# Optimization experiments

Measured on AMD Instinct MI355X. Metric: run time of the kernel, lower is better.

Reference implementation:

```python
import jax, jax.numpy as jnp
import numpy as np

PAD = 8192          # padding index == bloom_filter_dim
H1, H2 = 512, 64
B, K, L = 32, 32, 128


def prelu(x, alpha):
    return jnp.where(x >= 0, x, alpha * x)


def embedding_bag_mean(w, idx):
    # EmbeddingBag(mode='mean', padding_idx=PAD): mean over non-padding entries
    emb = w[idx]                                   # [..., L, H1]
    m = (idx != PAD)[..., None].astype(w.dtype)    # [..., L, 1]
    s = (emb * m).sum(axis=-2)
    cnt = m.sum(axis=-2)
    return jnp.where(cnt > 0, s / jnp.maximum(cnt, 1.0), 0.0)


def hidden_layers(x, W1, b1, W2, b2, a0, a1, a2):
    # PReLU -> Linear -> PReLU -> Linear -> PReLU
    h = prelu(x, a0)
    h = prelu(h @ W1 + b1, a1)
    h = prelu(h @ W2 + b2, a2)
    return h


def setup_inputs() -> dict:
    key = jax.random.key(0)
    ks = jax.random.split(key, 16)
    f = lambda i, shape: jax.random.normal(ks[i], shape, dtype=jnp.float32) * 0.05
    s = lambda v: jnp.asarray(v, dtype=jnp.float32)
    return {
        'query_bloom_filter': jax.random.randint(ks[0], (B, L), 0, PAD),
        'poi_bloom_filter': jax.random.randint(ks[1], (B, K, L), 0, PAD),
        'query_loc': jax.random.normal(ks[2], (B, 2), dtype=jnp.float32),
        'poi_loc': jax.random.normal(ks[3], (B, K, 2), dtype=jnp.float32),
        'codebook_w': f(4, (PAD + 1, H1)),
        'q_W1': f(5, (H1, H2)), 'q_b1': f(6, (H2,)),
        'q_W2': f(7, (H2, H2)), 'q_b2': f(8, (H2,)),
        'p_W1': f(9, (H1, H2)), 'p_b1': f(10, (H2,)),
        'p_W2': f(11, (H2, H2)), 'p_b2': f(12, (H2,)),
        'q_eval_w': f(13, (PAD + 1, H2)),
        'p_eval_w': f(14, (PAD + 1, H2)),
        'q_a0': s(0.25), 'q_a1': s(0.25), 'q_a2': s(0.25),
        'p_a0': s(0.25), 'p_a1': s(0.25), 'p_a2': s(0.25),
        'ind_a': s(0.25),
        'a': s(1.0), 'b': s(0.0), 'c': s(1.0), 'd': s(0.0),
    }


def reference(query_bloom_filter, poi_bloom_filter, query_loc, poi_loc,
              codebook_w, q_W1, q_b1, q_W2, q_b2, p_W1, p_b1, p_W2, p_b2,
              q_eval_w, p_eval_w, q_a0, q_a1, q_a2, p_a0, p_a1, p_a2,
              ind_a, a, b, c, d):
    # --- dense towers ---
    query_embedding = embedding_bag_mean(codebook_w, query_bloom_filter)      # [B, H1]
    query_hidden = hidden_layers(query_embedding, q_W1, q_b1, q_W2, q_b2,
                                 q_a0, q_a1, q_a2)                            # [B, H2]
    poi_embedding = embedding_bag_mean(codebook_w, poi_bloom_filter)          # [B, K, H1]
    poi_hidden = hidden_layers(poi_embedding, p_W1, p_b1, p_W2, p_b2,
                               p_a0, p_a1, p_a2)                              # [B, K, H2]

    # --- bloom-filter intersection (isin_cuda): q element present in poi set ---
    q = query_bloom_filter[:, None, :]                                        # [B, 1, L]
    p = poi_bloom_filter                                                      # [B, K, L]
    match = (q[..., :, None] == p[..., None, :]) & (p[..., None, :] != PAD)   # [B, K, L, L]
    intersection_mask = match.any(axis=-1)                                    # [B, K, L]
    intersection = jnp.where(intersection_mask, q, PAD)                       # [B, K, L]

    # --- sparse term weights via evaluator gathers + mul-sum ---
    q_cols = q_eval_w[intersection]                                           # [B, K, L, H2]
    p_cols = p_eval_w[intersection]                                           # [B, K, L, H2]
    q_sw = prelu(jnp.einsum('bh,bklh->bkl', query_hidden, q_cols), ind_a) + 1.0
    p_sw = prelu(jnp.einsum('bkh,bklh->bkl', poi_hidden, p_cols), ind_a) + 1.0

    text_sim = jnp.where(intersection_mask, q_sw * p_sw, 0.0).sum(axis=-1)    # [B, K]

    # --- location similarity ---
    dist = jnp.sqrt(((query_loc[:, None, :] - poi_loc) ** 2).sum(axis=-1))    # [B, K]
    dist_sim = -jnp.log(dist + 1.0)

    # --- text-sim normalization + relevance ---
    max_sim = text_sim.max(axis=-1, keepdims=True)
    text_sim = (2.0 * text_sim - max_sim) / (max_sim + 1e-6)
    relevance_score = (c - jax.nn.sigmoid(a * text_sim + b)) * (dist_sim - d)
    return relevance_score
```

## Files before the change

kernel.cpp:

```cpp
#include <hip/hip_runtime.h>

#define PAD_V 8192
#define H1 512
#define H2 64
#define B_SZ 32
#define K_SZ 32
#define L_SZ 128
#define NBAGS (B_SZ + B_SZ * K_SZ)
#define NSLICE 8
#define GATHER_BLOCKS (NBAGS * NSLICE)
#define ISECT2_BLOCKS ((B_SZ * K_SZ) / 2)


__global__ __launch_bounds__(256, 4) void gather_kernel(
    const int* __restrict__ qbf, const int* __restrict__ pbf,
    const float* __restrict__ codebook,
    const float* __restrict__ qa0p, const float* __restrict__ pa0p,
    float* __restrict__ x_ws,
    int* __restrict__ nh_ws, int* __restrict__ hits_ws)
{
    const int tid = threadIdx.x;

    if (blockIdx.x >= GATHER_BLOCKS) {
        __shared__ unsigned int bm2[2][256];
        __shared__ int s_nh2[2];
        __shared__ int s_hit2[2][L_SZ];

        const int pair0 = (blockIdx.x - GATHER_BLOCKS) * 2;
        const int sub = tid >> 7;
        const int t   = tid & 127;
        const int pair = pair0 + sub;
        const int b = pair >> 5;

        bm2[sub][t] = 0u; bm2[sub][t + 128] = 0u;
        if (t == 0) s_nh2[sub] = 0;
        __syncthreads();

        int pv = pbf[pair * L_SZ + t];
        if ((unsigned)pv < (unsigned)PAD_V)
            atomicOr(&bm2[sub][pv >> 5], 1u << (pv & 31));
        __syncthreads();

        int v = qbf[b * L_SZ + t];
        bool hit = ((unsigned)v < (unsigned)PAD_V) &&
                   ((bm2[sub][v >> 5] >> (v & 31)) & 1u);
        if (hit) {
            int pos = atomicAdd(&s_nh2[sub], 1);
            s_hit2[sub][pos] = v;
        }
        __syncthreads();

        if (t == 0) nh_ws[pair] = s_nh2[sub];
        if (t < s_nh2[sub]) hits_ws[pair * L_SZ + t] = s_hit2[sub][t];
        return;
    }

    const int slice = blockIdx.x & (NSLICE - 1);
    const int bag   = blockIdx.x >> 3;
    const bool is_q = (bag < B_SZ);
    const int* idx_base = is_q ? qbf : pbf;
    const int  bagl     = is_q ? bag : (bag - B_SZ);
    const float a0      = is_q ? *qa0p : *pa0p;

    __shared__ int   s_idx[L_SZ];
    __shared__ int   s_cnt[2];
    __shared__ float4 s_part[16][16];

    if (tid < L_SZ) {
        int v = idx_base[bagl * L_SZ + tid];
        s_idx[tid] = v;
        unsigned long long bal = __ballot(v != PAD_V);
        if ((tid & 63) == 0) s_cnt[tid >> 6] = __popcll(bal);
    }
    __syncthreads();

    const int c  = tid & 15;
    const int r0 = tid >> 4;
    const int gc = slice * 16 + c;
    const float4* cb4 = (const float4*)codebook;

    float ax = 0.f, ay = 0.f, az = 0.f, aw = 0.f;
    {
        int    idx[8];
        float4 buf[8];
        #pragma unroll
        for (int j = 0; j < 8; j++) idx[j] = s_idx[r0 * 8 + j];
        #pragma unroll
        for (int j = 0; j < 8; j++) buf[j] = cb4[(size_t)idx[j] * 128 + gc];
        #pragma unroll
        for (int j = 0; j < 8; j++) {
            float m = (idx[j] != PAD_V) ? 1.0f : 0.0f;
            ax = fmaf(m, buf[j].x, ax);
            ay = fmaf(m, buf[j].y, ay);
            az = fmaf(m, buf[j].z, az);
            aw = fmaf(m, buf[j].w, aw);
        }
    }
    s_part[r0][c] = make_float4(ax, ay, az, aw);
    __syncthreads();

    if (tid < 16) {
        int cnt = s_cnt[0] + s_cnt[1];
        float inv = (cnt > 0) ? 1.0f / (float)cnt : 0.0f;
        float e0 = 0.f, e1 = 0.f, e2 = 0.f, e3 = 0.f;
        #pragma unroll
        for (int r = 0; r < 16; r++) {
            float4 p = s_part[r][tid];
            e0 += p.x; e1 += p.y; e2 += p.z; e3 += p.w;
        }
        e0 *= inv; e1 *= inv; e2 *= inv; e3 *= inv;
        float4 o;
        o.x = (e0 >= 0.f) ? e0 : a0 * e0;
        o.y = (e1 >= 0.f) ? e1 : a0 * e1;
        o.z = (e2 >= 0.f) ? e2 : a0 * e2;
        o.w = (e3 >= 0.f) ? e3 : a0 * e3;
        ((float4*)x_ws)[(size_t)bag * 128 + slice * 16 + tid] = o;
    }
}

__global__ __launch_bounds__(256, 8) void mlp_kernel(
    const float* __restrict__ x_ws,
    const float* __restrict__ qW1, const float* __restrict__ qb1,
    const float* __restrict__ qW2, const float* __restrict__ qb2,
    const float* __restrict__ pW1, const float* __restrict__ pb1,
    const float* __restrict__ pW2, const float* __restrict__ pb2,
    const float* __restrict__ qa1p, const float* __restrict__ qa2p,
    const float* __restrict__ pa1p, const float* __restrict__ pa2p,
    float* __restrict__ qh_out, float* __restrict__ ph_out)
{
    const int tid = threadIdx.x;
    const int bag = blockIdx.x;
    const bool is_q = (bag < B_SZ);
    const float *W1, *b1, *W2, *b2;
    float a1, a2;
    float* out;
    int bagl;
    if (is_q) {
        bagl = bag;
        W1 = qW1; b1 = qb1; W2 = qW2; b2 = qb2;
        a1 = *qa1p; a2 = *qa2p;
        out = qh_out;
    } else {
        bagl = bag - B_SZ;
        W1 = pW1; b1 = pb1; W2 = pW2; b2 = pb2;
        a1 = *pa1p; a2 = *pa2p;
        out = ph_out;
    }

    __shared__ float s_x[H1];
    __shared__ float s_p1[16][H2];
    __shared__ float s_h1[H2];

    if (tid < 128)
        ((float4*)s_x)[tid] = ((const float4*)x_ws)[(size_t)bag * 128 + tid];
    __syncthreads();

    const int j4 = tid & 15;
    const int ch = tid >> 4;

    {
        const float4* W1v = (const float4*)W1;
        const int i0 = ch * 32;
        float sx = 0.f, sy = 0.f, sz = 0.f, sw = 0.f;
        #pragma unroll 8
        for (int i = 0; i < 32; i++) {
            float x = s_x[i0 + i];
            float4 w = W1v[(size_t)(i0 + i) * 16 + j4];
            sx = fmaf(x, w.x, sx);
            sy = fmaf(x, w.y, sy);
            sz = fmaf(x, w.z, sz);
            sw = fmaf(x, w.w, sw);
        }
        s_p1[ch][4 * j4 + 0] = sx;
        s_p1[ch][4 * j4 + 1] = sy;
        s_p1[ch][4 * j4 + 2] = sz;
        s_p1[ch][4 * j4 + 3] = sw;
    }
    __syncthreads();
    if (tid < H2) {
        float s = b1[tid];
        #pragma unroll
        for (int r = 0; r < 16; r++) s += s_p1[r][tid];
        s_h1[tid] = (s >= 0.f) ? s : a1 * s;
    }
    __syncthreads();

    {
        const float4* W2v = (const float4*)W2;
        const int i0 = ch * 4;
        float sx = 0.f, sy = 0.f, sz = 0.f, sw = 0.f;
        #pragma unroll
        for (int i = 0; i < 4; i++) {
            float x = s_h1[i0 + i];
            float4 w = W2v[(size_t)(i0 + i) * 16 + j4];
            sx = fmaf(x, w.x, sx);
            sy = fmaf(x, w.y, sy);
            sz = fmaf(x, w.z, sz);
            sw = fmaf(x, w.w, sw);
        }
        s_p1[ch][4 * j4 + 0] = sx;
        s_p1[ch][4 * j4 + 1] = sy;
        s_p1[ch][4 * j4 + 2] = sz;
        s_p1[ch][4 * j4 + 3] = sw;
    }
    __syncthreads();
    if (tid < H2) {
        float s = b2[tid];
        #pragma unroll
        for (int r = 0; r < 16; r++) s += s_p1[r][tid];
        s = (s >= 0.f) ? s : a2 * s;
        out[bagl * H2 + tid] = s;
    }
}

__global__ __launch_bounds__(64) void text_sim_kernel(
    const float* __restrict__ q_eval, const float* __restrict__ p_eval,
    const float* __restrict__ qh_ws, const float* __restrict__ ph_ws,
    const int* __restrict__ nh_ws, const int* __restrict__ hits_ws,
    const float* __restrict__ ind_ap,
    float* __restrict__ text_out)
{
    const int blk = blockIdx.x;
    const int b    = blk >> 5;
    const int lane = threadIdx.x;

    const float qh = qh_ws[b * H2 + lane];
    const float ph = ph_ws[blk * H2 + lane];
    const int   nh = nh_ws[blk];
    const float ind_a = *ind_ap;

    float local = 0.f;
    for (int hh = 0; hh < nh; hh++) {
        int v = hits_ws[blk * L_SZ + hh];
        float qd = qh * q_eval[(size_t)v * H2 + lane];
        float pd = ph * p_eval[(size_t)v * H2 + lane];
        #pragma unroll
        for (int m = 1; m < 64; m <<= 1) {
            qd += __shfl_xor(qd, m);
            pd += __shfl_xor(pd, m);
        }
        qd = (qd >= 0.f) ? qd : ind_a * qd;
        pd = (pd >= 0.f) ? pd : ind_a * pd;
        local += (qd + 1.f) * (pd + 1.f);
    }
    if (lane == 0) text_out[blk] = local;
}

__global__ __launch_bounds__(64) void epilogue_kernel(
    const float* __restrict__ text_ws,
    const float* __restrict__ qloc, const float* __restrict__ ploc,
    const float* __restrict__ ap, const float* __restrict__ bp,
    const float* __restrict__ cp, const float* __restrict__ dp,
    float* __restrict__ out)
{
    const int b = blockIdx.x;
    const int t = threadIdx.x;
    const int kk = t & 31;

    float ts_raw = text_ws[b * K_SZ + kk];
    float mx = ts_raw;
    #pragma unroll
    for (int m = 1; m < 32; m <<= 1) mx = fmaxf(mx, __shfl_xor(mx, m));

    float qx = qloc[b * 2], qy = qloc[b * 2 + 1];
    float px = ploc[(b * K_SZ + kk) * 2];
    float py = ploc[(b * K_SZ + kk) * 2 + 1];
    float dx = qx - px, dy = qy - py;
    float dist = sqrtf(dx * dx + dy * dy);
    float ds = -logf(dist + 1.0f);

    float ts = (2.0f * ts_raw - mx) / (mx + 1e-6f);
    float A = *ap, Bb = *bp, C = *cp, D = *dp;
    float sig = 1.0f / (1.0f + expf(-(A * ts + Bb)));
    if (t < 32) out[b * K_SZ + kk] = (C - sig) * (ds - D);
}

extern "C" void kernel_launch(void* const* d_in, const int* in_sizes, int n_in,
                              void* d_out, int out_size, void* d_ws, size_t ws_size,
                              hipStream_t stream) {
    const int*   qbf      = (const int*)d_in[0];
    const int*   pbf      = (const int*)d_in[1];
    const float* qloc     = (const float*)d_in[2];
    const float* ploc     = (const float*)d_in[3];
    const float* codebook = (const float*)d_in[4];
    const float* qW1      = (const float*)d_in[5];
    const float* qb1      = (const float*)d_in[6];
    const float* qW2      = (const float*)d_in[7];
    const float* qb2      = (const float*)d_in[8];
    const float* pW1      = (const float*)d_in[9];
    const float* pb1      = (const float*)d_in[10];
    const float* pW2      = (const float*)d_in[11];
    const float* pb2      = (const float*)d_in[12];
    const float* q_eval   = (const float*)d_in[13];
    const float* p_eval   = (const float*)d_in[14];
    const float* qa0      = (const float*)d_in[15];
    const float* qa1      = (const float*)d_in[16];
    const float* qa2      = (const float*)d_in[17];
    const float* pa0      = (const float*)d_in[18];
    const float* pa1      = (const float*)d_in[19];
    const float* pa2      = (const float*)d_in[20];
    const float* ind_a    = (const float*)d_in[21];
    const float* a        = (const float*)d_in[22];
    const float* bsc      = (const float*)d_in[23];
    const float* c        = (const float*)d_in[24];
    const float* d        = (const float*)d_in[25];

    float* qh   = (float*)d_ws;
    float* ph   = qh + B_SZ * H2;
    float* text = ph + B_SZ * K_SZ * H2;
    int*   nh   = (int*)(text + B_SZ * K_SZ);
    int*   hits = nh + B_SZ * K_SZ;
    float* x_ws = (float*)(hits + B_SZ * K_SZ * L_SZ);

    gather_kernel<<<GATHER_BLOCKS + ISECT2_BLOCKS, 256, 0, stream>>>(
        qbf, pbf, codebook, qa0, pa0, x_ws, nh, hits);

    mlp_kernel<<<NBAGS, 256, 0, stream>>>(
        x_ws, qW1, qb1, qW2, qb2, pW1, pb1, pW2, pb2,
        qa1, qa2, pa1, pa2, qh, ph);

    text_sim_kernel<<<B_SZ * K_SZ, 64, 0, stream>>>(
        q_eval, p_eval, qh, ph, nh, hits, ind_a, text);

    epilogue_kernel<<<B_SZ, 64, 0, stream>>>(
        text, qloc, ploc, a, bsc, c, d, (float*)d_out);
}
```

Baseline: 145.2 us.

## Batch four bags per MLP block, move intersection into MLP kernel, prefetch eval rows

The MLP kernel now handles four bags per block, so each W1/W2 row load is reused across four inputs instead of one. This cuts weight traffic and the block count. The bloom-filter intersection blocks move from the gather kernel into the MLP launch, and the text-sim loop software-prefetches the next hit's evaluator rows to hide gather latency. The cost is more shared memory and registers per MLP block, and the launch bound drops to 4 blocks per CU.

```diff
diff --git a/kernel.cpp b/kernel.cpp
--- a/kernel.cpp
+++ b/kernel.cpp
@@ -9,6 +9,7 @@
 #define NBAGS (B_SZ + B_SZ * K_SZ)
 #define NSLICE 8
 #define GATHER_BLOCKS (NBAGS * NSLICE)
+#define MLP4_BLOCKS (NBAGS / 4)
 #define ISECT2_BLOCKS ((B_SZ * K_SZ) / 2)
 
 
@@ -16,45 +17,9 @@
     const int* __restrict__ qbf, const int* __restrict__ pbf,
     const float* __restrict__ codebook,
     const float* __restrict__ qa0p, const float* __restrict__ pa0p,
-    float* __restrict__ x_ws,
-    int* __restrict__ nh_ws, int* __restrict__ hits_ws)
+    float* __restrict__ x_ws)
 {
     const int tid = threadIdx.x;
-
-    if (blockIdx.x >= GATHER_BLOCKS) {
-        __shared__ unsigned int bm2[2][256];
-        __shared__ int s_nh2[2];
-        __shared__ int s_hit2[2][L_SZ];
-
-        const int pair0 = (blockIdx.x - GATHER_BLOCKS) * 2;
-        const int sub = tid >> 7;
-        const int t   = tid & 127;
-        const int pair = pair0 + sub;
-        const int b = pair >> 5;
-
-        bm2[sub][t] = 0u; bm2[sub][t + 128] = 0u;
-        if (t == 0) s_nh2[sub] = 0;
-        __syncthreads();
-
-        int pv = pbf[pair * L_SZ + t];
-        if ((unsigned)pv < (unsigned)PAD_V)
-            atomicOr(&bm2[sub][pv >> 5], 1u << (pv & 31));
-        __syncthreads();
-
-        int v = qbf[b * L_SZ + t];
-        bool hit = ((unsigned)v < (unsigned)PAD_V) &&
-                   ((bm2[sub][v >> 5] >> (v & 31)) & 1u);
-        if (hit) {
-            int pos = atomicAdd(&s_nh2[sub], 1);
-            s_hit2[sub][pos] = v;
-        }
-        __syncthreads();
-
-        if (t == 0) nh_ws[pair] = s_nh2[sub];
-        if (t < s_nh2[sub]) hits_ws[pair * L_SZ + t] = s_hit2[sub][t];
-        return;
-    }
-
     const int slice = blockIdx.x & (NSLICE - 1);
     const int bag   = blockIdx.x >> 3;
     const bool is_q = (bag < B_SZ);
@@ -118,41 +83,83 @@
     }
 }
 
-__global__ __launch_bounds__(256, 8) void mlp_kernel(
+__global__ __launch_bounds__(256, 4) void mlp_isect_kernel(
     const float* __restrict__ x_ws,
+    const int* __restrict__ qbf, const int* __restrict__ pbf,
     const float* __restrict__ qW1, const float* __restrict__ qb1,
     const float* __restrict__ qW2, const float* __restrict__ qb2,
     const float* __restrict__ pW1, const float* __restrict__ pb1,
     const float* __restrict__ pW2, const float* __restrict__ pb2,
     const float* __restrict__ qa1p, const float* __restrict__ qa2p,
     const float* __restrict__ pa1p, const float* __restrict__ pa2p,
-    float* __restrict__ qh_out, float* __restrict__ ph_out)
+    float* __restrict__ qh_out, float* __restrict__ ph_out,
+    int* __restrict__ nh_ws, int* __restrict__ hits_ws)
 {
     const int tid = threadIdx.x;
-    const int bag = blockIdx.x;
-    const bool is_q = (bag < B_SZ);
+
+    if (blockIdx.x >= MLP4_BLOCKS) {
+        __shared__ unsigned int bm2[2][256];
+        __shared__ int s_nh2[2];
+        __shared__ int s_hit2[2][L_SZ];
+
+        const int pair0 = (blockIdx.x - MLP4_BLOCKS) * 2;
+        const int sub = tid >> 7;
+        const int t   = tid & 127;
+        const int pair = pair0 + sub;
+        const int b = pair >> 5;
+
+        bm2[sub][t] = 0u; bm2[sub][t + 128] = 0u;
+        if (t == 0) s_nh2[sub] = 0;
+        __syncthreads();
+
+        int pv = pbf[pair * L_SZ + t];
+        if ((unsigned)pv < (unsigned)PAD_V)
+            atomicOr(&bm2[sub][pv >> 5], 1u << (pv & 31));
+        __syncthreads();
+
+        int v = qbf[b * L_SZ + t];
+        bool hit = ((unsigned)v < (unsigned)PAD_V) &&
+                   ((bm2[sub][v >> 5] >> (v & 31)) & 1u);
+        if (hit) {
+            int pos = atomicAdd(&s_nh2[sub], 1);
+            s_hit2[sub][pos] = v;
+        }
+        __syncthreads();
+
+        if (t == 0) nh_ws[pair] = s_nh2[sub];
+        if (t < s_nh2[sub]) hits_ws[pair * L_SZ + t] = s_hit2[sub][t];
+        return;
+    }
+
+    const int m = blockIdx.x;
+    const bool is_q = (m < (B_SZ / 4));
+    const int bag0 = m * 4;
     const float *W1, *b1, *W2, *b2;
     float a1, a2;
     float* out;
-    int bagl;
+    int bagl0;
     if (is_q) {
-        bagl = bag;
+        bagl0 = bag0;
         W1 = qW1; b1 = qb1; W2 = qW2; b2 = qb2;
         a1 = *qa1p; a2 = *qa2p;
         out = qh_out;
     } else {
-        bagl = bag - B_SZ;
+        bagl0 = bag0 - B_SZ;
         W1 = pW1; b1 = pb1; W2 = pW2; b2 = pb2;
         a1 = *pa1p; a2 = *pa2p;
         out = ph_out;
     }
 
-    __shared__ float s_x[H1];
-    __shared__ float s_p1[16][H2];
-    __shared__ float s_h1[H2];
-
-    if (tid < 128)
-        ((float4*)s_x)[tid] = ((const float4*)x_ws)[(size_t)bag * 128 + tid];
+    __shared__ float s_x[4][H1];
+    __shared__ float s_p1[4][16][H2];
+    __shared__ float s_h1[4][H2];
+
+    {
+        const float4* x4 = (const float4*)x_ws;
+        float4* sx4 = (float4*)&s_x[0][0];
+        sx4[tid]       = x4[(size_t)bag0 * 128 + tid];
+        sx4[tid + 256] = x4[(size_t)bag0 * 128 + tid + 256];
+    }
     __syncthreads();
 
     const int j4 = tid & 15;
@@ -161,55 +168,85 @@
     {
         const float4* W1v = (const float4*)W1;
         const int i0 = ch * 32;
-        float sx = 0.f, sy = 0.f, sz = 0.f, sw = 0.f;
+        float4 A0 = make_float4(0.f,0.f,0.f,0.f);
+        float4 A1 = make_float4(0.f,0.f,0.f,0.f);
+        float4 A2 = make_float4(0.f,0.f,0.f,0.f);
+        float4 A3 = make_float4(0.f,0.f,0.f,0.f);
         #pragma unroll 8
         for (int i = 0; i < 32; i++) {
-            float x = s_x[i0 + i];
             float4 w = W1v[(size_t)(i0 + i) * 16 + j4];
-            sx = fmaf(x, w.x, sx);
-            sy = fmaf(x, w.y, sy);
-            sz = fmaf(x, w.z, sz);
-            sw = fmaf(x, w.w, sw);
-        }
-        s_p1[ch][4 * j4 + 0] = sx;
-        s_p1[ch][4 * j4 + 1] = sy;
-        s_p1[ch][4 * j4 + 2] = sz;
-        s_p1[ch][4 * j4 + 3] = sw;
-    }
-    __syncthreads();
-    if (tid < H2) {
-        float s = b1[tid];
-        #pragma unroll
-        for (int r = 0; r < 16; r++) s += s_p1[r][tid];
-        s_h1[tid] = (s >= 0.f) ? s : a1 * s;
+            float x0 = s_x[0][i0 + i];
+            float x1 = s_x[1][i0 + i];
+            float x2 = s_x[2][i0 + i];
+            float x3 = s_x[3][i0 + i];
+            A0.x = fmaf(x0, w.x, A0.x); A0.y = fmaf(x0, w.y, A0.y);
+            A0.z = fmaf(x0, w.z, A0.z); A0.w = fmaf(x0, w.w, A0.w);
+            A1.x = fmaf(x1, w.x, A1.x); A1.y = fmaf(x1, w.y, A1.y);
+            A1.z = fmaf(x1, w.z, A1.z); A1.w = fmaf(x1, w.w, A1.w);
+            A2.x = fmaf(x2, w.x, A2.x); A2.y = fmaf(x2, w.y, A2.y);
+            A2.z = fmaf(x2, w.z, A2.z); A2.w = fmaf(x2, w.w, A2.w);
+            A3.x = fmaf(x3, w.x, A3.x); A3.y = fmaf(x3, w.y, A3.y);
+            A3.z = fmaf(x3, w.z, A3.z); A3.w = fmaf(x3, w.w, A3.w);
+        }
+        s_p1[0][ch][4*j4+0] = A0.x; s_p1[0][ch][4*j4+1] = A0.y;
+        s_p1[0][ch][4*j4+2] = A0.z; s_p1[0][ch][4*j4+3] = A0.w;
+        s_p1[1][ch][4*j4+0] = A1.x; s_p1[1][ch][4*j4+1] = A1.y;
+        s_p1[1][ch][4*j4+2] = A1.z; s_p1[1][ch][4*j4+3] = A1.w;
+        s_p1[2][ch][4*j4+0] = A2.x; s_p1[2][ch][4*j4+1] = A2.y;
+        s_p1[2][ch][4*j4+2] = A2.z; s_p1[2][ch][4*j4+3] = A2.w;
+        s_p1[3][ch][4*j4+0] = A3.x; s_p1[3][ch][4*j4+1] = A3.y;
+        s_p1[3][ch][4*j4+2] = A3.z; s_p1[3][ch][4*j4+3] = A3.w;
+    }
+    __syncthreads();
+    {
+        const int bg = tid >> 6, col = tid & 63;
+        float s = b1[col];
+        #pragma unroll
+        for (int r = 0; r < 16; r++) s += s_p1[bg][r][col];
+        s_h1[bg][col] = (s >= 0.f) ? s : a1 * s;
     }
     __syncthreads();
 
     {
         const float4* W2v = (const float4*)W2;
         const int i0 = ch * 4;
-        float sx = 0.f, sy = 0.f, sz = 0.f, sw = 0.f;
+        float4 A0 = make_float4(0.f,0.f,0.f,0.f);
+        float4 A1 = make_float4(0.f,0.f,0.f,0.f);
+        float4 A2 = make_float4(0.f,0.f,0.f,0.f);
+        float4 A3 = make_float4(0.f,0.f,0.f,0.f);
         #pragma unroll
         for (int i = 0; i < 4; i++) {
-            float x = s_h1[i0 + i];
             float4 w = W2v[(size_t)(i0 + i) * 16 + j4];
-            sx = fmaf(x, w.x, sx);
-            sy = fmaf(x, w.y, sy);
-            sz = fmaf(x, w.z, sz);
-            sw = fmaf(x, w.w, sw);
-        }
-        s_p1[ch][4 * j4 + 0] = sx;
-        s_p1[ch][4 * j4 + 1] = sy;
-        s_p1[ch][4 * j4 + 2] = sz;
-        s_p1[ch][4 * j4 + 3] = sw;
-    }
-    __syncthreads();
-    if (tid < H2) {
-        float s = b2[tid];
-        #pragma unroll
-        for (int r = 0; r < 16; r++) s += s_p1[r][tid];
+            float x0 = s_h1[0][i0 + i];
+            float x1 = s_h1[1][i0 + i];
+            float x2 = s_h1[2][i0 + i];
+            float x3 = s_h1[3][i0 + i];
+            A0.x = fmaf(x0, w.x, A0.x); A0.y = fmaf(x0, w.y, A0.y);
+            A0.z = fmaf(x0, w.z, A0.z); A0.w = fmaf(x0, w.w, A0.w);
+            A1.x = fmaf(x1, w.x, A1.x); A1.y = fmaf(x1, w.y, A1.y);
+            A1.z = fmaf(x1, w.z, A1.z); A1.w = fmaf(x1, w.w, A1.w);
+            A2.x = fmaf(x2, w.x, A2.x); A2.y = fmaf(x2, w.y, A2.y);
+            A2.z = fmaf(x2, w.z, A2.z); A2.w = fmaf(x2, w.w, A2.w);
+            A3.x = fmaf(x3, w.x, A3.x); A3.y = fmaf(x3, w.y, A3.y);
+            A3.z = fmaf(x3, w.z, A3.z); A3.w = fmaf(x3, w.w, A3.w);
+        }
+        s_p1[0][ch][4*j4+0] = A0.x; s_p1[0][ch][4*j4+1] = A0.y;
+        s_p1[0][ch][4*j4+2] = A0.z; s_p1[0][ch][4*j4+3] = A0.w;
+        s_p1[1][ch][4*j4+0] = A1.x; s_p1[1][ch][4*j4+1] = A1.y;
+        s_p1[1][ch][4*j4+2] = A1.z; s_p1[1][ch][4*j4+3] = A1.w;
+        s_p1[2][ch][4*j4+0] = A2.x; s_p1[2][ch][4*j4+1] = A2.y;
+        s_p1[2][ch][4*j4+2] = A2.z; s_p1[2][ch][4*j4+3] = A2.w;
+        s_p1[3][ch][4*j4+0] = A3.x; s_p1[3][ch][4*j4+1] = A3.y;
+        s_p1[3][ch][4*j4+2] = A3.z; s_p1[3][ch][4*j4+3] = A3.w;
+    }
+    __syncthreads();
+    {
+        const int bg = tid >> 6, col = tid & 63;
+        float s = b2[col];
+        #pragma unroll
+        for (int r = 0; r < 16; r++) s += s_p1[bg][r][col];
         s = (s >= 0.f) ? s : a2 * s;
-        out[bagl * H2 + tid] = s;
+        out[(bagl0 + bg) * H2 + col] = s;
     }
 }
 
@@ -230,18 +267,29 @@
     const float ind_a = *ind_ap;
 
     float local = 0.f;
-    for (int hh = 0; hh < nh; hh++) {
-        int v = hits_ws[blk * L_SZ + hh];
-        float qd = qh * q_eval[(size_t)v * H2 + lane];
-        float pd = ph * p_eval[(size_t)v * H2 + lane];
-        #pragma unroll
-        for (int m = 1; m < 64; m <<= 1) {
-            qd += __shfl_xor(qd, m);
-            pd += __shfl_xor(pd, m);
-        }
-        qd = (qd >= 0.f) ? qd : ind_a * qd;
-        pd = (pd >= 0.f) ? pd : ind_a * pd;
-        local += (qd + 1.f) * (pd + 1.f);
+    if (nh > 0) {
+        int v = hits_ws[blk * L_SZ];
+        float qe = q_eval[(size_t)v * H2 + lane];
+        float pe = p_eval[(size_t)v * H2 + lane];
+        for (int hh = 0; hh < nh; hh++) {
+            float qe_n = 0.f, pe_n = 0.f;
+            if (hh + 1 < nh) {
+                int vn = hits_ws[blk * L_SZ + hh + 1];
+                qe_n = q_eval[(size_t)vn * H2 + lane];
+                pe_n = p_eval[(size_t)vn * H2 + lane];
+            }
+            float qd = qh * qe;
+            float pd = ph * pe;
+            #pragma unroll
+            for (int m = 1; m < 64; m <<= 1) {
+                qd += __shfl_xor(qd, m);
+                pd += __shfl_xor(pd, m);
+            }
+            qd = (qd >= 0.f) ? qd : ind_a * qd;
+            pd = (pd >= 0.f) ? pd : ind_a * pd;
+            local += (qd + 1.f) * (pd + 1.f);
+            qe = qe_n; pe = pe_n;
+        }
     }
     if (lane == 0) text_out[blk] = local;
 }
@@ -312,12 +360,13 @@
     int*   hits = nh + B_SZ * K_SZ;
     float* x_ws = (float*)(hits + B_SZ * K_SZ * L_SZ);
 
-    gather_kernel<<<GATHER_BLOCKS + ISECT2_BLOCKS, 256, 0, stream>>>(
-        qbf, pbf, codebook, qa0, pa0, x_ws, nh, hits);
-
-    mlp_kernel<<<NBAGS, 256, 0, stream>>>(
-        x_ws, qW1, qb1, qW2, qb2, pW1, pb1, pW2, pb2,
-        qa1, qa2, pa1, pa2, qh, ph);
+    gather_kernel<<<GATHER_BLOCKS, 256, 0, stream>>>(
+        qbf, pbf, codebook, qa0, pa0, x_ws);
+
+    mlp_isect_kernel<<<MLP4_BLOCKS + ISECT2_BLOCKS, 256, 0, stream>>>(
+        x_ws, qbf, pbf,
+        qW1, qb1, qW2, qb2, pW1, pb1, pW2, pb2,
+        qa1, qa2, pa1, pa2, qh, ph, nh, hits);
 
     text_sim_kernel<<<B_SZ * K_SZ, 64, 0, stream>>>(
         q_eval, p_eval, qh, ph, nh, hits, ind_a, text);
```

After: 139.4 us, median of 2. 4.0% less time.
